# Optimization experiments

Measured on AMD Instinct MI355X. Metric: run time of the kernel, lower is better.

## Reference

```python
import jax, jax.numpy as jnp
import numpy as np

N_NODES = 100000
NUM_ETYPE = 4
HEADS = 4
HID = 32
IN_CH = 128
EDGE_CH = 32
N_EDGES = 800000
BATCH = 1024
NEG = 5


def setup_inputs() -> dict:
    key = jax.random.key(0)
    ks = jax.random.split(key, 24)

    def w(k, shape, s=0.05):
        return jax.random.normal(k, shape, dtype=jnp.float32) * s

    inp = {}
    inp["edge_index"] = jax.random.randint(ks[0], (2, N_EDGES), 0, N_NODES)
    inp["edge_type"] = jax.random.randint(ks[1], (N_EDGES,), 0, NUM_ETYPE)
    inp["n_id"] = jax.random.randint(ks[2], (BATCH * (2 + NEG),), 0, N_NODES)
    inp["neg_sample_num"] = NEG
    inp["id_emb"] = w(ks[3], (N_NODES, IN_CH), 0.1)
    dims = [IN_CH, HEADS * HID]
    for i in range(2):
        d_in = dims[i]
        base = 4 + i * 7
        inp[f"W{i}"] = w(ks[base], (d_in, HEADS * HID))
        inp[f"Wres{i}"] = w(ks[base + 1], (d_in, HEADS * HID))
        inp[f"al{i}"] = w(ks[base + 2], (HEADS, HID))
        inp[f"ar{i}"] = w(ks[base + 3], (HEADS, HID))
        inp[f"ae{i}"] = w(ks[base + 4], (HEADS, EDGE_CH))
        inp[f"eemb{i}"] = w(ks[base + 5], (NUM_ETYPE, EDGE_CH))
        inp[f"We{i}"] = w(ks[base + 6], (EDGE_CH, HEADS * EDGE_CH))
    inp["pW1"] = w(ks[18], (2 * HEADS * HID, HID))
    inp["pb1"] = jnp.zeros((HID,), jnp.float32)
    inp["pW2"] = w(ks[19], (HID, 1))
    inp["pb2"] = jnp.zeros((1,), jnp.float32)
    return inp


def _leaky(x):
    return jnp.where(x > 0, x, 0.2 * x)  # LeakyReLU(0.2)


def _conv(h, src, dst, etype, W, Wres, al, ar, ae, eemb, We):
    """Simple-HGN style edge-typed graph attention conv with linear residual."""
    n = h.shape[0]
    feat = (h @ W).reshape(n, HEADS, HID)                      # [N,H,D]
    ef = (eemb @ We).reshape(NUM_ETYPE, HEADS, EDGE_CH)        # [T,H,De]
    el = jnp.einsum('nhd,hd->nh', feat, al)                    # [N,H]
    er = jnp.einsum('nhd,hd->nh', feat, ar)                    # [N,H]
    ee = jnp.einsum('thd,hd->th', ef, ae)                      # [T,H]
    logits = _leaky(el[src] + er[dst] + ee[etype])             # [E,H]
    # numerically stable per-destination softmax over incoming edges
    m = jax.ops.segment_max(logits, dst, num_segments=n)
    m = jnp.where(jnp.isfinite(m), m, jnp.zeros_like(m))
    a = jnp.exp(logits - m[dst])
    denom = jax.ops.segment_sum(a, dst, num_segments=n)
    alpha = a / (denom[dst] + 1e-16)                           # [E,H]
    out = jax.ops.segment_sum(feat[src] * alpha[:, :, None], dst, num_segments=n)
    return out.reshape(n, HEADS * HID) + h @ Wres


def reference(edge_index, edge_type, n_id, neg_sample_num, id_emb,
              W0, Wres0, al0, ar0, ae0, eemb0, We0,
              W1, Wres1, al1, ar1, ae1, eemb1, We1,
              pW1, pb1, pW2, pb2):
    src, dst = edge_index[0], edge_index[1]
    x = _conv(id_emb, src, dst, edge_type, W0, Wres0, al0, ar0, ae0, eemb0, We0)
    x = jax.nn.relu(x)  # relu between layers; dropout inactive at eval
    x = _conv(x, src, dst, edge_type, W1, Wres1, al1, ar1, ae1, eemb1, We1)
    b = n_id.shape[0] // (2 + neg_sample_num)
    out = x[n_id[:b]]
    pos = x[n_id[b:2 * b]]
    neg = x[n_id[2 * b:]]
    tiled = jnp.repeat(out, neg_sample_num, axis=0)  # repeat(1,neg).reshape(-1,D)

    def head(z):
        return _leaky(z @ pW1 + pb1) @ pW2 + pb2

    pos_logit = head(jnp.concatenate([out, pos], axis=-1))
    neg_logits = head(jnp.concatenate([tiled, neg], axis=-1))
    return pos_logit, neg_logits
```

## Files before the change

### kernel.cpp

```cpp
#include <hip/hip_runtime.h>
#include <hip/hip_bf16.h>
#include <math.h>

#define HEADS 4
#define HID 32
#define DIM 128
#define NEGS 5

typedef short s16x8 __attribute__((ext_vector_type(8)));
typedef short s16x4 __attribute__((ext_vector_type(4)));
typedef unsigned short u16x8 __attribute__((ext_vector_type(8)));
typedef float f32x4 __attribute__((ext_vector_type(4)));

__device__ __forceinline__ unsigned short f2bf_rn(float x) {
    unsigned int u = __float_as_uint(x);
    unsigned int r = (u + 0x7FFFu + ((u >> 16) & 1u)) >> 16;
    return (unsigned short)r;
}
__device__ __forceinline__ float bf2f(unsigned short b) {
    return __uint_as_float(((unsigned int)b) << 16);
}

__global__ void k_histflag(const int* __restrict__ src, const int* __restrict__ dst,
                           const int* __restrict__ flag2,
                           int* __restrict__ counts, int* __restrict__ flag1, int E) {
    int e = blockIdx.x * 256 + threadIdx.x;
    if (e < E) {
        int d = dst[e];
        atomicAdd(&counts[d], 1);
        if (flag2[d]) flag1[src[e]] = 1;
    }
}

__global__ __launch_bounds__(1024) void k_scanA(const int* __restrict__ counts,
                                                int* __restrict__ rowtmp,
                                                int* __restrict__ bsum, int N) {
    __shared__ int s[1024];
    int i = blockIdx.x * 1024 + threadIdx.x;
    int v = (i < N) ? counts[i] : 0;
    s[threadIdx.x] = v;
    __syncthreads();
    for (int off = 1; off < 1024; off <<= 1) {
        int t = (threadIdx.x >= off) ? s[threadIdx.x - off] : 0;
        __syncthreads();
        s[threadIdx.x] += t;
        __syncthreads();
    }
    if (i < N) rowtmp[i] = s[threadIdx.x];
    if (threadIdx.x == 1023) bsum[blockIdx.x] = s[1023];
}

__global__ void k_scanB(const int* __restrict__ bsum, int* __restrict__ bsumex, int nb) {
    int l = threadIdx.x;
    int a = (2 * l < nb) ? bsum[2 * l] : 0;
    int b = (2 * l + 1 < nb) ? bsum[2 * l + 1] : 0;
    int s = a + b;
    for (int off = 1; off < 64; off <<= 1) {
        int t = __shfl_up(s, off);
        if (l >= off) s += t;
    }
    int excl = s - (a + b);
    if (2 * l < nb) bsumex[2 * l] = excl;
    if (2 * l + 1 < nb) bsumex[2 * l + 1] = excl + a;
}

__global__ void k_scanC(const int* __restrict__ rowtmp, const int* __restrict__ counts,
                        const int* __restrict__ bsumex, int* __restrict__ row_start,
                        int* __restrict__ cursor, int N) {
    int i = blockIdx.x * 256 + threadIdx.x;
    if (i < N) {
        int st = rowtmp[i] - counts[i] + bsumex[i >> 10];
        row_start[i] = st;
        cursor[i] = st;
    }
}

__global__ void k_scatter(const int* __restrict__ dst, int* __restrict__ cursor,
                          int* __restrict__ csr_edge, int E) {
    int e = blockIdx.x * 256 + threadIdx.x;
    if (e < E) {
        int p = atomicAdd(&cursor[dst[e]], 1);
        csr_edge[p] = e;
    }
}

__global__ void k_flag2(const int* __restrict__ n_id, int* __restrict__ flag2,
                        int* __restrict__ flag1, int M) {
    int i = blockIdx.x * 256 + threadIdx.x;
    if (i < M) { int n = n_id[i]; flag2[n] = 1; flag1[n] = 1; }
}

__global__ void k_compact(const int* __restrict__ flag1, const int* __restrict__ flag2,
                          int* __restrict__ list1, int* __restrict__ list2,
                          int* __restrict__ cnt1, int* __restrict__ cnt2, int N) {
    int i = blockIdx.x * 256 + threadIdx.x;
    int lane = threadIdx.x & 63;
    unsigned long long lt = (lane == 63) ? ~0ull >> 1 : (1ull << lane) - 1;

    bool a = (i < N) && flag1[i];
    unsigned long long m = __ballot(a);
    int base = 0;
    if (lane == 0 && m) base = atomicAdd(cnt1, __popcll(m));
    base = __shfl(base, 0);
    if (a) list1[base + __popcll(m & lt)] = i;

    bool b = (i < N) && flag2[i];
    m = __ballot(b);
    base = 0;
    if (lane == 0 && m) base = atomicAdd(cnt2, __popcll(m));
    base = __shfl(base, 0);
    if (b) list2[base + __popcll(m & lt)] = i;
}

__global__ void k_wcvt(const float* __restrict__ W0, const float* __restrict__ Wres0,
                       const float* __restrict__ W1, const float* __restrict__ Wres1,
                       unsigned short* __restrict__ bt) {
    int idx = blockIdx.x * 256 + threadIdx.x;
    int layer = idx >> 15;
    int r = idx & 32767;
    int k = r >> 8;
    int n = r & 255;
    const float* src = layer ? ((n < 128) ? W1 : Wres1) : ((n < 128) ? W0 : Wres0);
    float x = src[k * 128 + (n & 127)];
    unsigned short h = f2bf_rn(x);
    unsigned short l = f2bf_rn(x - bf2f(h));
    unsigned short* base = bt + (size_t)layer * 2 * 32768;
    base[n * 128 + k] = h;
    base[32768 + n * 128 + k] = l;
}

__global__ void k_acvt(const float* __restrict__ A, unsigned short* __restrict__ Ahi,
                       unsigned short* __restrict__ Alo, int N) {
    int t = blockIdx.x * 256 + threadIdx.x;
    if (t >= N * 16) return;
    int row = t >> 4, part = t & 15, ks = part >> 2, g = part & 3;
    const float* ap = A + (size_t)row * DIM + ks * 32 + g * 4;
    float4 p = *(const float4*)ap;
    float4 q = *(const float4*)(ap + 16);
    float vv[8] = {p.x, p.y, p.z, p.w, q.x, q.y, q.z, q.w};
    u16x8 hv, lv;
#pragma unroll
    for (int j = 0; j < 8; ++j) {
        unsigned short h = f2bf_rn(vv[j]);
        hv[j] = h;
        lv[j] = f2bf_rn(vv[j] - bf2f(h));
    }
    size_t o = (size_t)row * DIM + ks * 32 + g * 8;
    *(u16x8*)(Ahi + o) = hv;
    *(u16x8*)(Alo + o) = lv;
}

template <int PRECONV>
__global__ __launch_bounds__(256, PRECONV ? 5 : 4)
void k_gemm_fused(const float* __restrict__ A,
                  const unsigned short* __restrict__ Aph,
                  const unsigned short* __restrict__ Apl,
                  const unsigned short* __restrict__ Bhi,
                  const unsigned short* __restrict__ Blo,
                  unsigned short* __restrict__ featb,
                  float* __restrict__ res,
                  const float* __restrict__ al,
                  const float* __restrict__ ar,
                  float* __restrict__ el,
                  float* __restrict__ er,
                  const int* __restrict__ rowlist,
                  const int* __restrict__ rowcnt,
                  const int* __restrict__ resflag,
                  int N) {
    int limit = rowcnt ? *rowcnt : N;
    int c = blockIdx.x;
    int m0 = blockIdx.y * 64;
    if (m0 >= limit) return;

    __shared__ unsigned short Bh[8192];
    __shared__ unsigned short Bl[8192];
    int tid = threadIdx.x;
    int lane = tid & 63, w = tid >> 6;
    int wm = (w & 1) * 32, wn = (w >> 1) * 32;
    int lr = lane & 15, g = lane >> 4;

#pragma unroll
    for (int i = 0; i < 4; ++i) {
        int f = tid + i * 256;
        int row = f >> 4, g16 = f & 15;
        int off = (row * 256 + ((g16 * 16) ^ ((row & 7) << 4))) >> 1;
        *(u16x8*)&Bh[off] = *(const u16x8*)(Bhi + (size_t)(c * 64 + row) * DIM + g16 * 8);
        *(u16x8*)&Bl[off] = *(const u16x8*)(Blo + (size_t)(c * 64 + row) * DIM + g16 * 8);
    }

    s16x8 afh[2][4], afl[2][4];
#pragma unroll
    for (int fm = 0; fm < 2; ++fm) {
        int idx = m0 + wm + fm * 16 + lr;
        bool valid = idx < limit;
        int grow = 0;
        if (valid) grow = rowlist ? rowlist[idx] : idx;
        if (PRECONV) {
            const unsigned short* hp = Aph + (size_t)grow * DIM;
            const unsigned short* lp = Apl + (size_t)grow * DIM;
#pragma unroll
            for (int ks = 0; ks < 4; ++ks) {
                if (valid) {
                    afh[fm][ks] = (s16x8)(*(const u16x8*)(hp + ks * 32 + g * 8));
                    afl[fm][ks] = (s16x8)(*(const u16x8*)(lp + ks * 32 + g * 8));
                } else {
                    afh[fm][ks] = (s16x8){0, 0, 0, 0, 0, 0, 0, 0};
                    afl[fm][ks] = (s16x8){0, 0, 0, 0, 0, 0, 0, 0};
                }
            }
        } else {
            const float* ap = A + (size_t)grow * DIM;
#pragma unroll
            for (int ks = 0; ks < 4; ++ks) {
                float4 p = make_float4(0.f, 0.f, 0.f, 0.f);
                float4 q = make_float4(0.f, 0.f, 0.f, 0.f);
                if (valid) {
                    p = *(const float4*)(ap + ks * 32 + g * 4);
                    q = *(const float4*)(ap + ks * 32 + 16 + g * 4);
                }
                float vv[8] = {p.x, p.y, p.z, p.w, q.x, q.y, q.z, q.w};
                s16x8 hv, lv;
#pragma unroll
                for (int j = 0; j < 8; ++j) {
                    unsigned short h = f2bf_rn(vv[j]);
                    hv[j] = (short)h;
                    lv[j] = (short)f2bf_rn(vv[j] - bf2f(h));
                }
                afh[fm][ks] = hv;
                afl[fm][ks] = lv;
            }
        }
    }
    __syncthreads();

    f32x4 acc[2][2];
#pragma unroll
    for (int fm = 0; fm < 2; ++fm)
#pragma unroll
        for (int fn = 0; fn < 2; ++fn) acc[fm][fn] = (f32x4){0.f, 0.f, 0.f, 0.f};

#pragma unroll
    for (int ks = 0; ks < 4; ++ks) {
        s16x8 bfh[2], bfl[2];
#pragma unroll
        for (int fn = 0; fn < 2; ++fn) {
            int row = wn + fn * 16 + lr;
            int sw = (row & 7) << 4;
            int o1 = (row * 256 + ((ks * 64 + g * 8) ^ sw)) >> 1;
            int o2 = (row * 256 + ((ks * 64 + 32 + g * 8) ^ sw)) >> 1;
            s16x4 p = *(const s16x4*)&Bh[o1];
            s16x4 q = *(const s16x4*)&Bh[o2];
            bfh[fn] = (s16x8){p[0], p[1], p[2], p[3], q[0], q[1], q[2], q[3]};
            p = *(const s16x4*)&Bl[o1];
            q = *(const s16x4*)&Bl[o2];
            bfl[fn] = (s16x8){p[0], p[1], p[2], p[3], q[0], q[1], q[2], q[3]};
        }
#pragma unroll
        for (int fm = 0; fm < 2; ++fm)
#pragma unroll
            for (int fn = 0; fn < 2; ++fn) {
                acc[fm][fn] = __builtin_amdgcn_mfma_f32_16x16x32_bf16(afh[fm][ks], bfh[fn], acc[fm][fn], 0, 0, 0);
                acc[fm][fn] = __builtin_amdgcn_mfma_f32_16x16x32_bf16(afh[fm][ks], bfl[fn], acc[fm][fn], 0, 0, 0);
                acc[fm][fn] = __builtin_amdgcn_mfma_f32_16x16x32_bf16(afl[fm][ks], bfh[fn], acc[fm][fn], 0, 0, 0);
            }
    }

#pragma unroll
    for (int fm = 0; fm < 2; ++fm)
#pragma unroll
        for (int fn = 0; fn < 2; ++fn) {
            int idx0 = m0 + wm + fm * 16 + g * 4;
            int dc = ((c * 64) & 127) + wn + fn * 16 + lr;
#pragma unroll
            for (int r = 0; r < 4; ++r) {
                int idx = idx0 + r;
                if (idx < limit) {
                    int gr = rowlist ? rowlist[idx] : idx;
                    if (c < 2) {
                        featb[(size_t)gr * DIM + dc] = f2bf_rn(acc[fm][fn][r]);
                    } else if (!resflag || resflag[gr]) {
                        res[(size_t)gr * DIM + dc] = acc[fm][fn][r];
                    }
                }
            }
        }

    if (c < 2) {
        int h = c * 2 + (wn >> 5);
        float a0 = al[h * HID + lr], a1 = al[h * HID + 16 + lr];
        float b0 = ar[h * HID + lr], b1 = ar[h * HID + 16 + lr];
#pragma unroll
        for (int fm = 0; fm < 2; ++fm)
#pragma unroll
            for (int r = 0; r < 4; ++r) {
                float ev = acc[fm][0][r] * a0 + acc[fm][1][r] * a1;
                float rv = acc[fm][0][r] * b0 + acc[fm][1][r] * b1;
#pragma unroll
                for (int off = 1; off < 16; off <<= 1) {
                    ev += __shfl_xor(ev, off);
                    rv += __shfl_xor(rv, off);
                }
                if (lr == 0) {
                    int idx = m0 + wm + fm * 16 + g * 4 + r;
                    if (idx < limit) {
                        int node = rowlist ? rowlist[idx] : idx;
                        el[node * 4 + h] = ev;
                        er[node * 4 + h] = rv;
                    }
                }
            }
    }
}

__global__ void k_ee(const float* __restrict__ eemb, const float* __restrict__ We,
                     const float* __restrict__ ae, float* __restrict__ ee) {
    int t = threadIdx.x;
    if (t >= 16) return;
    int et = t >> 2, h = t & 3;
    float s = 0.f;
    for (int d = 0; d < 32; ++d) {
        float ef = 0.f;
        for (int k = 0; k < 32; ++k) ef += eemb[et * 32 + k] * We[k * DIM + h * 32 + d];
        s += ef * ae[h * 32 + d];
    }
    ee[t] = s;
}

template <int RELU>
__global__ __launch_bounds__(256) void k_agg(const unsigned short* __restrict__ featb,
                                             const float* __restrict__ el,
                                             const float* __restrict__ er,
                                             const float* __restrict__ eeB,
                                             const int* __restrict__ srcArr,
                                             const int* __restrict__ etArr,
                                             const int* __restrict__ csr_edge,
                                             const int* __restrict__ row_start,
                                             const int* __restrict__ counts,
                                             const int* __restrict__ dlist,
                                             const int* __restrict__ dcnt,
                                             float* __restrict__ out) {
    int wv = threadIdx.x >> 6;
    int lane = threadIdx.x & 63;
    int idx = blockIdx.x * 4 + wv;
    if (idx >= *dcnt) return;
    int node = dlist[idx];

    int beg = row_start[node];
    int deg = counts[node];
    int eh = lane & 3;
    float er_v = er[node * 4 + eh];

    float m = -INFINITY;
    for (int base = 0; base < deg; base += 16) {
        int ei = base + (lane >> 2);
        float lg = -INFINITY;
        if (ei < deg) {
            int e = csr_edge[beg + ei];
            float x = el[srcArr[e] * 4 + eh] + er_v + eeB[etArr[e] * 4 + eh];
            lg = (x > 0.f) ? x : 0.2f * x;
        }
        m = fmaxf(m, lg);
    }
    for (int off = 4; off < 64; off <<= 1) m = fmaxf(m, __shfl_xor(m, off));

    float denom = 0.f, acc0 = 0.f, acc1 = 0.f;
    int h1 = lane >> 5;
    for (int base = 0; base < deg; base += 16) {
        int ei = base + (lane >> 2);
        float wgt = 0.f;
        int s = 0;
        if (ei < deg) {
            int e = csr_edge[beg + ei];
            s = srcArr[e];
            float x = el[s * 4 + eh] + er_v + eeB[etArr[e] * 4 + eh];
            x = (x > 0.f) ? x : 0.2f * x;
            wgt = expf(x - m);
            denom += wgt;
        }
        int cnt = min(16, deg - base);
        for (int j = 0; j < cnt; ++j) {
            int sj = __shfl(s, j * 4);
            float w1 = __shfl(wgt, j * 4 + h1);
            float w2 = __shfl(wgt, j * 4 + 2 + h1);
            acc0 += w1 * bf2f(featb[(size_t)sj * DIM + lane]);
            acc1 += w2 * bf2f(featb[(size_t)sj * DIM + 64 + lane]);
        }
    }
    for (int off = 4; off < 64; off <<= 1) denom += __shfl_xor(denom, off);
    float d1 = __shfl(denom, h1);
    float d2 = __shfl(denom, 2 + h1);

    float r0 = out[(size_t)node * DIM + lane] + acc0 / (d1 + 1e-16f);
    float r1 = out[(size_t)node * DIM + 64 + lane] + acc1 / (d2 + 1e-16f);
    if (RELU) { r0 = fmaxf(r0, 0.f); r1 = fmaxf(r1, 0.f); }
    out[(size_t)node * DIM + lane] = r0;
    out[(size_t)node * DIM + 64 + lane] = r1;
}

__global__ __launch_bounds__(256) void k_head(const float* __restrict__ x1,
                                              const int* __restrict__ n_id,
                                              const float* __restrict__ pW1,
                                              const float* __restrict__ pb1,
                                              const float* __restrict__ pW2,
                                              const float* __restrict__ pb2,
                                              float* __restrict__ dout, int B) {
    int o = blockIdx.x * 4 + (threadIdx.x >> 6);
    int lane = threadIdx.x & 63;
    int total = B + B * NEGS;
    if (o >= total) return;
    int a, c;
    if (o < B) { a = n_id[o]; c = n_id[B + o]; }
    else { int j = o - B; a = n_id[j / NEGS]; c = n_id[2 * B + j]; }

    int j = lane & 31;
    int half = lane >> 5;
    int row = half ? c : a;
    const float* z = x1 + (size_t)row * DIM;
    const float* w = pW1 + (half ? 128 * 32 : 0);
    float t = 0.f;
#pragma unroll 8
    for (int k = 0; k < 128; ++k) t += z[k] * w[k * 32 + j];
    t += __shfl_xor(t, 32);
    t += pb1[j];
    t = (t > 0.f) ? t : 0.2f * t;
    float r = t * pW2[j];
    for (int off = 1; off < 32; off <<= 1) r += __shfl_xor(r, off);
    if (lane == 0) dout[o] = r + pb2[0];
}

extern "C" void kernel_launch(void* const* d_in, const int* in_sizes, int n_in,
                              void* d_out, int out_size, void* d_ws, size_t ws_size,
                              hipStream_t stream) {
    const int* edge_index = (const int*)d_in[0];
    const int* etype      = (const int*)d_in[1];
    const int* n_id       = (const int*)d_in[2];
    const float* id_emb   = (const float*)d_in[4];
    const float* W0    = (const float*)d_in[5];
    const float* Wres0 = (const float*)d_in[6];
    const float* al0   = (const float*)d_in[7];
    const float* ar0   = (const float*)d_in[8];
    const float* ae0   = (const float*)d_in[9];
    const float* eemb0 = (const float*)d_in[10];
    const float* We0   = (const float*)d_in[11];
    const float* W1    = (const float*)d_in[12];
    const float* Wres1 = (const float*)d_in[13];
    const float* al1   = (const float*)d_in[14];
    const float* ar1   = (const float*)d_in[15];
    const float* ae1   = (const float*)d_in[16];
    const float* eemb1 = (const float*)d_in[17];
    const float* We1   = (const float*)d_in[18];
    const float* pW1   = (const float*)d_in[19];
    const float* pb1   = (const float*)d_in[20];
    const float* pW2   = (const float*)d_in[21];
    const float* pb2   = (const float*)d_in[22];

    int E = in_sizes[1];
    int N = in_sizes[4] / DIM;
    int M = in_sizes[2];
    int B = M / (2 + NEGS);
    const int* srcArr = edge_index;
    const int* dstArr = edge_index + E;

    size_t N128 = (size_t)N * DIM;
    unsigned short* featb = (unsigned short*)d_ws;
    unsigned short* Ahi   = featb + N128;
    unsigned short* Alo   = Ahi + N128;
    float* x1   = (float*)Ahi;
    float* x0   = (float*)(Alo + N128);
    float* el   = x0 + N128;
    float* er   = el + (size_t)N * 4;
    float* eeB  = er + (size_t)N * 4;
    int* counts    = (int*)(eeB + 32);
    int* flag1     = counts + N;
    int* flag2     = flag1 + N;
    int* cnt1      = flag2 + N;
    int* cnt2      = cnt1 + 1;
    int* rowtmp    = cnt2 + 1;
    int* row_start = rowtmp + N;
    int* cursor    = row_start + N;
    int* csr_edge  = cursor + N;
    int* list1     = csr_edge + E;
    int* list2     = list1 + N;
    int* bsum      = list2 + M;
    int* bsumex    = bsum + 256;
    unsigned short* bt = (unsigned short*)(bsumex + 256);

    k_wcvt<<<256, 256, 0, stream>>>(W0, Wres0, W1, Wres1, bt);
    k_acvt<<<(N * 16 + 255) / 256, 256, 0, stream>>>(id_emb, Ahi, Alo, N);
    hipMemsetAsync(counts, 0, (size_t)(3 * N + 2) * sizeof(int), stream);

    k_flag2<<<(M + 255) / 256, 256, 0, stream>>>(n_id, flag2, flag1, M);
    k_histflag<<<(E + 255) / 256, 256, 0, stream>>>(srcArr, dstArr, flag2, counts, flag1, E);

    int nb = (N + 1023) / 1024;
    k_scanA<<<nb, 1024, 0, stream>>>(counts, rowtmp, bsum, N);
    k_scanB<<<1, 64, 0, stream>>>(bsum, bsumex, nb);
    k_scanC<<<(N + 255) / 256, 256, 0, stream>>>(rowtmp, counts, bsumex, row_start, cursor, N);
    k_scatter<<<(E + 255) / 256, 256, 0, stream>>>(dstArr, cursor, csr_edge, E);
    k_compact<<<(N + 255) / 256, 256, 0, stream>>>(flag1, flag2, list1, list2, cnt1, cnt2, N);

    dim3 ggrid(4, (N + 63) / 64);
    int aggGridFull = (N + 3) / 4;
    int aggGridS2 = (M + 3) / 4;

    k_gemm_fused<1><<<ggrid, 256, 0, stream>>>(nullptr, Ahi, Alo, bt, bt + 32768,
                                               featb, x0, al0, ar0, el, er,
                                               nullptr, nullptr, flag1, N);
    k_ee<<<1, 16, 0, stream>>>(eemb0, We0, ae0, eeB);
    k_agg<1><<<aggGridFull, 256, 0, stream>>>(featb, el, er, eeB, srcArr, etype, csr_edge,
                                              row_start, counts, list1, cnt1, x0);

    k_gemm_fused<0><<<ggrid, 256, 0, stream>>>(x0, nullptr, nullptr, bt + 65536, bt + 98304,
                                               featb, x1, al1, ar1, el, er,
                                               list1, cnt1, flag2, N);
    k_ee<<<1, 16, 0, stream>>>(eemb1, We1, ae1, eeB);
    k_agg<0><<<aggGridS2, 256, 0, stream>>>(featb, el, er, eeB, srcArr, etype, csr_edge,
                                            row_start, counts, list2, cnt2, x1);

    int total = B * (1 + NEGS);
    k_head<<<(total + 3) / 4, 256, 0, stream>>>(x1, n_id, pW1, pb1, pW2, pb2,
                                                (float*)d_out, B);
}
```

Measured before the change: 397.8 us.

## Make fused GEMM persistent so each block reuses its LDS B tile across rows

The fused GEMM is turned into a persistent kernel. Each block loads its 64-column B slice into shared memory once, then loops over row tiles with a grid-stride loop. The grid is cut to about a third of the row blocks, and the al/ar loads are hoisted out of the loop. This amortizes the B-tile load and block launch overhead, but it gives up the early exit for row blocks past the live count in layer two and lowers PRECONV occupancy bounds from 5 to 4.

New measurement: 494.8 us. 24.4% more time.

```diff
diff --git a/kernel.cpp b/kernel.cpp
--- a/kernel.cpp
+++ b/kernel.cpp
@@ -151,26 +151,25 @@
 }
 
 template <int PRECONV>
-__global__ __launch_bounds__(256, PRECONV ? 5 : 4)
-void k_gemm_fused(const float* __restrict__ A,
-                  const unsigned short* __restrict__ Aph,
-                  const unsigned short* __restrict__ Apl,
-                  const unsigned short* __restrict__ Bhi,
-                  const unsigned short* __restrict__ Blo,
-                  unsigned short* __restrict__ featb,
-                  float* __restrict__ res,
-                  const float* __restrict__ al,
-                  const float* __restrict__ ar,
-                  float* __restrict__ el,
-                  float* __restrict__ er,
-                  const int* __restrict__ rowlist,
-                  const int* __restrict__ rowcnt,
-                  const int* __restrict__ resflag,
-                  int N) {
+__global__ __launch_bounds__(256, 4)
+void k_gemm_pers(const float* __restrict__ A,
+                 const unsigned short* __restrict__ Aph,
+                 const unsigned short* __restrict__ Apl,
+                 const unsigned short* __restrict__ Bhi,
+                 const unsigned short* __restrict__ Blo,
+                 unsigned short* __restrict__ featb,
+                 float* __restrict__ res,
+                 const float* __restrict__ al,
+                 const float* __restrict__ ar,
+                 float* __restrict__ el,
+                 float* __restrict__ er,
+                 const int* __restrict__ rowlist,
+                 const int* __restrict__ rowcnt,
+                 const int* __restrict__ resflag,
+                 int N) {
     int limit = rowcnt ? *rowcnt : N;
     int c = blockIdx.x;
-    int m0 = blockIdx.y * 64;
-    if (m0 >= limit) return;
+    int nTiles = (limit + 63) >> 6;
 
     __shared__ unsigned short Bh[8192];
     __shared__ unsigned short Bl[8192];
@@ -187,128 +186,138 @@
         *(u16x8*)&Bh[off] = *(const u16x8*)(Bhi + (size_t)(c * 64 + row) * DIM + g16 * 8);
         *(u16x8*)&Bl[off] = *(const u16x8*)(Blo + (size_t)(c * 64 + row) * DIM + g16 * 8);
     }
-
-    s16x8 afh[2][4], afl[2][4];
-#pragma unroll
-    for (int fm = 0; fm < 2; ++fm) {
-        int idx = m0 + wm + fm * 16 + lr;
-        bool valid = idx < limit;
-        int grow = 0;
-        if (valid) grow = rowlist ? rowlist[idx] : idx;
-        if (PRECONV) {
-            const unsigned short* hp = Aph + (size_t)grow * DIM;
-            const unsigned short* lp = Apl + (size_t)grow * DIM;
-#pragma unroll
-            for (int ks = 0; ks < 4; ++ks) {
-                if (valid) {
-                    afh[fm][ks] = (s16x8)(*(const u16x8*)(hp + ks * 32 + g * 8));
-                    afl[fm][ks] = (s16x8)(*(const u16x8*)(lp + ks * 32 + g * 8));
-                } else {
-                    afh[fm][ks] = (s16x8){0, 0, 0, 0, 0, 0, 0, 0};
-                    afl[fm][ks] = (s16x8){0, 0, 0, 0, 0, 0, 0, 0};
+    __syncthreads();
+
+    int h = c * 2 + (wn >> 5);
+    float a0 = 0.f, a1 = 0.f, b0 = 0.f, b1 = 0.f;
+    if (c < 2) {
+        a0 = al[h * HID + lr]; a1 = al[h * HID + 16 + lr];
+        b0 = ar[h * HID + lr]; b1 = ar[h * HID + 16 + lr];
+    }
+
+    for (int t = blockIdx.y; t < nTiles; t += gridDim.y) {
+        int m0 = t * 64;
+
+        s16x8 afh[2][4], afl[2][4];
+        int grows[2];
+#pragma unroll
+        for (int fm = 0; fm < 2; ++fm) {
+            int idx = m0 + wm + fm * 16 + lr;
+            bool valid = idx < limit;
+            int grow = 0;
+            if (valid) grow = rowlist ? rowlist[idx] : idx;
+            grows[fm] = grow;
+            if (PRECONV) {
+                const unsigned short* hp = Aph + (size_t)grow * DIM;
+                const unsigned short* lp = Apl + (size_t)grow * DIM;
+#pragma unroll
+                for (int ks = 0; ks < 4; ++ks) {
+                    if (valid) {
+                        afh[fm][ks] = (s16x8)(*(const u16x8*)(hp + ks * 32 + g * 8));
+                        afl[fm][ks] = (s16x8)(*(const u16x8*)(lp + ks * 32 + g * 8));
+                    } else {
+                        afh[fm][ks] = (s16x8){0, 0, 0, 0, 0, 0, 0, 0};
+                        afl[fm][ks] = (s16x8){0, 0, 0, 0, 0, 0, 0, 0};
+                    }
+                }
+            } else {
+                const float* ap = A + (size_t)grow * DIM;
+#pragma unroll
+                for (int ks = 0; ks < 4; ++ks) {
+                    float4 p = make_float4(0.f, 0.f, 0.f, 0.f);
+                    float4 q = make_float4(0.f, 0.f, 0.f, 0.f);
+                    if (valid) {
+                        p = *(const float4*)(ap + ks * 32 + g * 4);
+                        q = *(const float4*)(ap + ks * 32 + 16 + g * 4);
+                    }
+                    float vv[8] = {p.x, p.y, p.z, p.w, q.x, q.y, q.z, q.w};
+                    s16x8 hv, lv;
+#pragma unroll
+                    for (int j = 0; j < 8; ++j) {
+                        unsigned short hh = f2bf_rn(vv[j]);
+                        hv[j] = (short)hh;
+                        lv[j] = (short)f2bf_rn(vv[j] - bf2f(hh));
+                    }
+                    afh[fm][ks] = hv;
+                    afl[fm][ks] = lv;
                 }
             }
-        } else {
-            const float* ap = A + (size_t)grow * DIM;
-#pragma unroll
-            for (int ks = 0; ks < 4; ++ks) {
-                float4 p = make_float4(0.f, 0.f, 0.f, 0.f);
-                float4 q = make_float4(0.f, 0.f, 0.f, 0.f);
-                if (valid) {
-                    p = *(const float4*)(ap + ks * 32 + g * 4);
-                    q = *(const float4*)(ap + ks * 32 + 16 + g * 4);
+        }
+
+        f32x4 acc[2][2];
+#pragma unroll
+        for (int fm = 0; fm < 2; ++fm)
+#pragma unroll
+            for (int fn = 0; fn < 2; ++fn) acc[fm][fn] = (f32x4){0.f, 0.f, 0.f, 0.f};
+
+#pragma unroll
+        for (int ks = 0; ks < 4; ++ks) {
+            s16x8 bfh[2], bfl[2];
+#pragma unroll
+            for (int fn = 0; fn < 2; ++fn) {
+                int row = wn + fn * 16 + lr;
+                int sw = (row & 7) << 4;
+                int o1 = (row * 256 + ((ks * 64 + g * 8) ^ sw)) >> 1;
+                int o2 = (row * 256 + ((ks * 64 + 32 + g * 8) ^ sw)) >> 1;
+                s16x4 p = *(const s16x4*)&Bh[o1];
+                s16x4 q = *(const s16x4*)&Bh[o2];
+                bfh[fn] = (s16x8){p[0], p[1], p[2], p[3], q[0], q[1], q[2], q[3]};
+                p = *(const s16x4*)&Bl[o1];
+                q = *(const s16x4*)&Bl[o2];
+                bfl[fn] = (s16x8){p[0], p[1], p[2], p[3], q[0], q[1], q[2], q[3]};
+            }
+#pragma unroll
+            for (int fm = 0; fm < 2; ++fm)
+#pragma unroll
+                for (int fn = 0; fn < 2; ++fn) {
+                    acc[fm][fn] = __builtin_amdgcn_mfma_f32_16x16x32_bf16(afh[fm][ks], bfh[fn], acc[fm][fn], 0, 0, 0);
+                    acc[fm][fn] = __builtin_amdgcn_mfma_f32_16x16x32_bf16(afh[fm][ks], bfl[fn], acc[fm][fn], 0, 0, 0);
+                    acc[fm][fn] = __builtin_amdgcn_mfma_f32_16x16x32_bf16(afl[fm][ks], bfh[fn], acc[fm][fn], 0, 0, 0);
                 }
-                float vv[8] = {p.x, p.y, p.z, p.w, q.x, q.y, q.z, q.w};
-                s16x8 hv, lv;
-#pragma unroll
-                for (int j = 0; j < 8; ++j) {
-                    unsigned short h = f2bf_rn(vv[j]);
-                    hv[j] = (short)h;
-                    lv[j] = (short)f2bf_rn(vv[j] - bf2f(h));
-                }
-                afh[fm][ks] = hv;
-                afl[fm][ks] = lv;
-            }
         }
-    }
-    __syncthreads();
-
-    f32x4 acc[2][2];
-#pragma unroll
-    for (int fm = 0; fm < 2; ++fm)
-#pragma unroll
-        for (int fn = 0; fn < 2; ++fn) acc[fm][fn] = (f32x4){0.f, 0.f, 0.f, 0.f};
-
-#pragma unroll
-    for (int ks = 0; ks < 4; ++ks) {
-        s16x8 bfh[2], bfl[2];
-#pragma unroll
-        for (int fn = 0; fn < 2; ++fn) {
-            int row = wn + fn * 16 + lr;
-            int sw = (row & 7) << 4;
-            int o1 = (row * 256 + ((ks * 64 + g * 8) ^ sw)) >> 1;
-            int o2 = (row * 256 + ((ks * 64 + 32 + g * 8) ^ sw)) >> 1;
-            s16x4 p = *(const s16x4*)&Bh[o1];
-            s16x4 q = *(const s16x4*)&Bh[o2];
-            bfh[fn] = (s16x8){p[0], p[1], p[2], p[3], q[0], q[1], q[2], q[3]};
-            p = *(const s16x4*)&Bl[o1];
-            q = *(const s16x4*)&Bl[o2];
-            bfl[fn] = (s16x8){p[0], p[1], p[2], p[3], q[0], q[1], q[2], q[3]};
-        }
+
 #pragma unroll
         for (int fm = 0; fm < 2; ++fm)
 #pragma unroll
             for (int fn = 0; fn < 2; ++fn) {
-                acc[fm][fn] = __builtin_amdgcn_mfma_f32_16x16x32_bf16(afh[fm][ks], bfh[fn], acc[fm][fn], 0, 0, 0);
-                acc[fm][fn] = __builtin_amdgcn_mfma_f32_16x16x32_bf16(afh[fm][ks], bfl[fn], acc[fm][fn], 0, 0, 0);
-                acc[fm][fn] = __builtin_amdgcn_mfma_f32_16x16x32_bf16(afl[fm][ks], bfh[fn], acc[fm][fn], 0, 0, 0);
-            }
-    }
-
-#pragma unroll
-    for (int fm = 0; fm < 2; ++fm)
-#pragma unroll
-        for (int fn = 0; fn < 2; ++fn) {
-            int idx0 = m0 + wm + fm * 16 + g * 4;
-            int dc = ((c * 64) & 127) + wn + fn * 16 + lr;
-#pragma unroll
-            for (int r = 0; r < 4; ++r) {
-                int idx = idx0 + r;
-                if (idx < limit) {
-                    int gr = rowlist ? rowlist[idx] : idx;
-                    if (c < 2) {
-                        featb[(size_t)gr * DIM + dc] = f2bf_rn(acc[fm][fn][r]);
-                    } else if (!resflag || resflag[gr]) {
-                        res[(size_t)gr * DIM + dc] = acc[fm][fn][r];
+                int idx0 = m0 + wm + fm * 16 + g * 4;
+                int dc = ((c * 64) & 127) + wn + fn * 16 + lr;
+#pragma unroll
+                for (int r = 0; r < 4; ++r) {
+                    int idx = idx0 + r;
+                    if (idx < limit) {
+                        int gr = rowlist ? rowlist[idx] : idx;
+                        if (c < 2) {
+                            featb[(size_t)gr * DIM + dc] = f2bf_rn(acc[fm][fn][r]);
+                        } else if (!resflag || resflag[gr]) {
+                            res[(size_t)gr * DIM + dc] = acc[fm][fn][r];
+                        }
                     }
                 }
             }
-        }
-
-    if (c < 2) {
-        int h = c * 2 + (wn >> 5);
-        float a0 = al[h * HID + lr], a1 = al[h * HID + 16 + lr];
-        float b0 = ar[h * HID + lr], b1 = ar[h * HID + 16 + lr];
-#pragma unroll
-        for (int fm = 0; fm < 2; ++fm)
-#pragma unroll
-            for (int r = 0; r < 4; ++r) {
-                float ev = acc[fm][0][r] * a0 + acc[fm][1][r] * a1;
-                float rv = acc[fm][0][r] * b0 + acc[fm][1][r] * b1;
-#pragma unroll
-                for (int off = 1; off < 16; off <<= 1) {
-                    ev += __shfl_xor(ev, off);
-                    rv += __shfl_xor(rv, off);
-                }
-                if (lr == 0) {
-                    int idx = m0 + wm + fm * 16 + g * 4 + r;
-                    if (idx < limit) {
-                        int node = rowlist ? rowlist[idx] : idx;
-                        el[node * 4 + h] = ev;
-                        er[node * 4 + h] = rv;
+
+        if (c < 2) {
+#pragma unroll
+            for (int fm = 0; fm < 2; ++fm)
+#pragma unroll
+                for (int r = 0; r < 4; ++r) {
+                    float ev = acc[fm][0][r] * a0 + acc[fm][1][r] * a1;
+                    float rv = acc[fm][0][r] * b0 + acc[fm][1][r] * b1;
+#pragma unroll
+                    for (int off = 1; off < 16; off <<= 1) {
+                        ev += __shfl_xor(ev, off);
+                        rv += __shfl_xor(rv, off);
+                    }
+                    if (lr == 0) {
+                        int idx = m0 + wm + fm * 16 + g * 4 + r;
+                        if (idx < limit) {
+                            int node = rowlist ? rowlist[idx] : idx;
+                            el[node * 4 + h] = ev;
+                            er[node * 4 + h] = rv;
+                        }
                     }
                 }
-            }
+        }
     }
 }
 
@@ -499,20 +508,22 @@
     k_scatter<<<(E + 255) / 256, 256, 0, stream>>>(dstArr, cursor, csr_edge, E);
     k_compact<<<(N + 255) / 256, 256, 0, stream>>>(flag1, flag2, list1, list2, cnt1, cnt2, N);
 
-    dim3 ggrid(4, (N + 63) / 64);
+    int nRowBlk = (N + 63) / 64;
+    int P = (nRowBlk + 2) / 3;
+    dim3 ggrid(4, P);
     int aggGridFull = (N + 3) / 4;
     int aggGridS2 = (M + 3) / 4;
 
-    k_gemm_fused<1><<<ggrid, 256, 0, stream>>>(nullptr, Ahi, Alo, bt, bt + 32768,
-                                               featb, x0, al0, ar0, el, er,
-                                               nullptr, nullptr, flag1, N);
+    k_gemm_pers<1><<<ggrid, 256, 0, stream>>>(nullptr, Ahi, Alo, bt, bt + 32768,
+                                              featb, x0, al0, ar0, el, er,
+                                              nullptr, nullptr, flag1, N);
     k_ee<<<1, 16, 0, stream>>>(eemb0, We0, ae0, eeB);
     k_agg<1><<<aggGridFull, 256, 0, stream>>>(featb, el, er, eeB, srcArr, etype, csr_edge,
                                               row_start, counts, list1, cnt1, x0);
 
-    k_gemm_fused<0><<<ggrid, 256, 0, stream>>>(x0, nullptr, nullptr, bt + 65536, bt + 98304,
-                                               featb, x1, al1, ar1, el, er,
-                                               list1, cnt1, flag2, N);
+    k_gemm_pers<0><<<ggrid, 256, 0, stream>>>(x0, nullptr, nullptr, bt + 65536, bt + 98304,
+                                              featb, x1, al1, ar1, el, er,
+                                              list1, cnt1, flag2, N);
     k_ee<<<1, 16, 0, stream>>>(eemb1, We1, ae1, eeB);
     k_agg<0><<<aggGridS2, 256, 0, stream>>>(featb, el, er, eeB, srcArr, etype, csr_edge,
                                             row_start, counts, list2, cnt2, x1);
```
